# Optimization experiments

Measured on AMD Instinct MI355X. Metric: run time of the kernel, lower is better.

## Reference

```python
import jax, jax.numpy as jnp
import numpy as np

EPS = 1e-10


def _gcn(X, A, W, act):
    # A_hat = A + I; symmetric normalization D^{-1/2} A_hat D^{-1/2}
    N = A.shape[0]
    A_hat = A + jnp.eye(N, dtype=A.dtype)
    d = 1.0 / jnp.sqrt(jnp.sum(A_hat, axis=1) + EPS)
    A_norm = (d[:, None] * A_hat) * d[None, :]  # same math as diag @ A_hat @ diag
    return act(A_norm @ (X @ W))


def _pool(X, A, s, k):
    scores = (X @ s)[:, 0]            # [N]
    _, idx = jax.lax.top_k(scores, k)  # static k (ceil(ratio*N))
    return X[idx], A[idx][:, idx], idx


def _unpool(Xp, idx, N):
    return jnp.zeros((N, Xp.shape[-1]), Xp.dtype).at[idx].set(Xp)


def _glorot(key, shape):
    lim = np.sqrt(6.0 / (shape[0] + shape[1])).astype(np.float32)
    return jax.random.uniform(key, shape, jnp.float32, -lim, lim)


def setup_inputs() -> dict:
    key = jax.random.key(0)
    ks = jax.random.split(key, 8)
    N, F_IN, F, C = 8192, 16, 32, 2
    x = jax.random.normal(ks[0], (N, F_IN), jnp.float32)
    # sparse-ish symmetric binary adjacency stored densely (as the module expects)
    a = (jax.random.uniform(ks[1], (N, N)) < 0.01).astype(jnp.float32)
    a = jnp.maximum(a, a.T)
    return {
        "x": x,
        "a": a,
        "W1": _glorot(ks[2], (F_IN, F)),
        "W2": _glorot(ks[3], (F, F)),
        "W3": _glorot(ks[4], (F, F)),
        "W4": _glorot(ks[5], (F, C)),
        "s1": _glorot(ks[6], (F, 1)),
        "s2": _glorot(ks[7], (F, 1)),
    }


def reference(x, a, W1, W2, W3, W4, s1, s2):
    N = x.shape[0]
    K1 = int(np.ceil(0.5 * N))   # pool1 ratio 0.5
    K2 = int(np.ceil(0.5 * K1))  # pool2 ratio 0.5
    relu = jax.nn.relu
    X1 = _gcn(x, a, W1, relu)                     # [N, F]
    X1p, A1p, idx1 = _pool(X1, a, s1, K1)         # [K1, F], [K1, K1]
    X2 = _gcn(X1p, A1p, W2, relu)                 # [K1, F]
    X2p, _, idx2 = _pool(X2, A1p, s2, K2)         # [K2, F]
    X3 = _unpool(X2p, idx2, K1)                   # scatter back to [K1, F]
    X3 = _gcn(X3, A1p, W3, relu)
    X4 = _unpool(X3, idx1, N)                     # scatter back to [N, F]
    return _gcn(X4, a, W4, lambda z: jax.nn.softmax(z, axis=-1))
```

## Files before the change

kernel.cpp:

```cpp
#include <hip/hip_runtime.h>
#include <stdint.h>

#define NNODES 8192
#define KP1 4096
#define KP2 2048
#define FIN 16
#define FH 32
#define COUT 2
#define STRA 320
#define STRS 320
#define CGRID 1024
#define GRPSH 5
#define GRPSZ 32
#define BARWORDS (66 * 32)
#define RNONE 0xFFFFu

typedef unsigned short u16;
typedef unsigned int u32;

__global__ __launch_bounds__(256) void build_ell(const float* __restrict__ A, int n, int stride,
        u16* __restrict__ ell, int* __restrict__ rowcnt, int* __restrict__ diag, float* __restrict__ dnorm,
        const float* __restrict__ Xf, const float* __restrict__ Wf, float* __restrict__ Zf, int kf,
        u32* __restrict__ bar)
{
    if ((int)blockIdx.x >= n) {
        if ((int)blockIdx.x == n) {
            for (int w = threadIdx.x; w < BARWORDS; w += 256)
                __hip_atomic_store(&bar[w], 0u, __ATOMIC_RELAXED, __HIP_MEMORY_SCOPE_AGENT);
        }
        int t = ((int)blockIdx.x - n) * 256 + threadIdx.x;
        int i = t >> 5;
        int f = t & 31;
        const float* xr = Xf + (size_t)i * kf;
        float acc = 0.0f;
        for (int k = 0; k < kf; ++k) acc += xr[k] * Wf[k * 32 + f];
        Zf[t] = acc;
        return;
    }
    __shared__ int cnt;
    __shared__ int dg;
    int row = blockIdx.x;
    if (threadIdx.x == 0) { cnt = 0; dg = 0; }
    __syncthreads();
    const float4* arow4 = (const float4*)(A + (size_t)row * n);
    u16* erow = ell + (size_t)row * stride;
    int n4 = n >> 2;
    for (int c4 = threadIdx.x; c4 < n4; c4 += 256) {
        float4 v = arow4[c4];
        if (v.x == 0.0f && v.y == 0.0f && v.z == 0.0f && v.w == 0.0f) continue;
        int cb = c4 << 2;
        if (v.x != 0.0f) {
            if (cb == row) dg = 1;
            else { int p = atomicAdd(&cnt, 1); if (p < stride) erow[p] = (u16)cb; }
        }
        if (v.y != 0.0f) {
            int c = cb + 1;
            if (c == row) dg = 1;
            else { int p = atomicAdd(&cnt, 1); if (p < stride) erow[p] = (u16)c; }
        }
        if (v.z != 0.0f) {
            int c = cb + 2;
            if (c == row) dg = 1;
            else { int p = atomicAdd(&cnt, 1); if (p < stride) erow[p] = (u16)c; }
        }
        if (v.w != 0.0f) {
            int c = cb + 3;
            if (c == row) dg = 1;
            else { int p = atomicAdd(&cnt, 1); if (p < stride) erow[p] = (u16)c; }
        }
    }
    __syncthreads();
    if (threadIdx.x == 0) {
        int cf = cnt;
        rowcnt[row] = cf < stride ? cf : stride;
        diag[row] = dg;
        dnorm[row] = rsqrtf((float)(cf + dg + 1) + 1e-10f);
    }
}

__device__ __forceinline__ void gbar(u32* bar, int bid, int nblk)
{
    __syncthreads();
    if (threadIdx.x == 0) {
        __builtin_amdgcn_fence(__ATOMIC_RELEASE, "agent");
        int g = bid >> GRPSH;
        int ngrp = (nblk + GRPSZ - 1) >> GRPSH;
        int gsz = nblk - (g << GRPSH); if (gsz > GRPSZ) gsz = GRPSZ;
        u32* gcnt = bar + (size_t)g * 32;
        u32* ggen = bar + (size_t)(32 + g) * 32;
        u32* rcnt = bar + (size_t)64 * 32;
        u32* rgen = bar + (size_t)65 * 32;
        u32 sg = __hip_atomic_load(ggen, __ATOMIC_RELAXED, __HIP_MEMORY_SCOPE_AGENT);
        u32 a = __hip_atomic_fetch_add(gcnt, 1u, __ATOMIC_RELAXED, __HIP_MEMORY_SCOPE_AGENT);
        if (a == (u32)(gsz - 1)) {
            u32 sr = __hip_atomic_load(rgen, __ATOMIC_RELAXED, __HIP_MEMORY_SCOPE_AGENT);
            u32 r = __hip_atomic_fetch_add(rcnt, 1u, __ATOMIC_RELAXED, __HIP_MEMORY_SCOPE_AGENT);
            if (r == (u32)(ngrp - 1)) {
                __hip_atomic_store(rcnt, 0u, __ATOMIC_RELAXED, __HIP_MEMORY_SCOPE_AGENT);
                __hip_atomic_fetch_add(rgen, 1u, __ATOMIC_RELAXED, __HIP_MEMORY_SCOPE_AGENT);
            } else {
                while (__hip_atomic_load(rgen, __ATOMIC_RELAXED, __HIP_MEMORY_SCOPE_AGENT) == sr)
                    __builtin_amdgcn_s_sleep(2);
            }
            __hip_atomic_store(gcnt, 0u, __ATOMIC_RELAXED, __HIP_MEMORY_SCOPE_AGENT);
            __hip_atomic_fetch_add(ggen, 1u, __ATOMIC_RELAXED, __HIP_MEMORY_SCOPE_AGENT);
        } else {
            while (__hip_atomic_load(ggen, __ATOMIC_RELAXED, __HIP_MEMORY_SCOPE_AGENT) == sg)
                __builtin_amdgcn_s_sleep(4);
        }
        __builtin_amdgcn_fence(__ATOMIC_ACQUIRE, "agent");
    }
    __syncthreads();
}

struct TkS {
    u32 hist[4][256];
    u32 wsum[4];
    u32 pref;
    u32 rem;
};

__device__ __forceinline__ u32 km_of(float f)
{
    u32 u = __float_as_uint(f);
    u32 m;
    if (u & 0x80000000u) m = ~u; else m = u | 0x80000000u;
    return ~m;
}

__device__ void topk_local(TkS& s, u16* rank_l, u16* idx_l,
                           const float* __restrict__ scores, int n, int K, int tid,
                           int* __restrict__ grank, int* __restrict__ gidx, bool mirror)
{
    int wv = tid >> 6;
    int lane = tid & 63;
    int per = n >> 8;
    int base = tid * per;
    if (tid == 0) { s.pref = 0u; s.rem = (u32)K; }
    __syncthreads();
    for (int bp = 3; bp >= 0; --bp) {
        s.hist[0][tid] = 0u;
        s.hist[1][tid] = 0u;
        s.hist[2][tid] = 0u;
        s.hist[3][tid] = 0u;
        __syncthreads();
        u32 maskhi = 0u;
        if (bp < 3) maskhi = 0xFFFFFFFFu << ((bp + 1) * 8);
        u32 pref = s.pref;
        u32 rem = s.rem;
        for (int e = 0; e < per; ++e) {
            u32 km = km_of(scores[base + e]);
            if ((km & maskhi) == pref) atomicAdd(&s.hist[wv][(km >> (bp * 8)) & 255u], 1u);
        }
        __syncthreads();
        u32 tot = s.hist[0][tid] + s.hist[1][tid] + s.hist[2][tid] + s.hist[3][tid];
        u32 vv = tot;
        u32 t2;
        t2 = __shfl(vv, lane - 1);  if (lane >= 1)  vv += t2;
        t2 = __shfl(vv, lane - 2);  if (lane >= 2)  vv += t2;
        t2 = __shfl(vv, lane - 4);  if (lane >= 4)  vv += t2;
        t2 = __shfl(vv, lane - 8);  if (lane >= 8)  vv += t2;
        t2 = __shfl(vv, lane - 16); if (lane >= 16) vv += t2;
        t2 = __shfl(vv, lane - 32); if (lane >= 32) vv += t2;
        if (lane == 63) s.wsum[wv] = vv;
        __syncthreads();
        u32 add = 0u;
        if (wv > 0) add += s.wsum[0];
        if (wv > 1) add += s.wsum[1];
        if (wv > 2) add += s.wsum[2];
        u32 cum = vv + add;
        if (tot != 0u && cum >= rem && cum - tot < rem) {
            s.pref = pref | ((u32)tid << (bp * 8));
            s.rem = rem - (cum - tot);
        }
    }
    __syncthreads();
    u32 T = s.pref;
    u32 need_eq = s.rem;
    u32 run = 0u;
    for (int e = 0; e < per; ++e) {
        u32 km = km_of(scores[base + e]);
        if (km < T) run += 0x10000u;
        else if (km == T) run += 1u;
    }
    u32 v2 = run;
    u32 t3;
    t3 = __shfl(v2, lane - 1);  if (lane >= 1)  v2 += t3;
    t3 = __shfl(v2, lane - 2);  if (lane >= 2)  v2 += t3;
    t3 = __shfl(v2, lane - 4);  if (lane >= 4)  v2 += t3;
    t3 = __shfl(v2, lane - 8);  if (lane >= 8)  v2 += t3;
    t3 = __shfl(v2, lane - 16); if (lane >= 16) v2 += t3;
    t3 = __shfl(v2, lane - 32); if (lane >= 32) v2 += t3;
    if (lane == 63) s.wsum[wv] = v2;
    __syncthreads();
    u32 add2 = 0u;
    if (wv > 0) add2 += s.wsum[0];
    if (wv > 1) add2 += s.wsum[1];
    if (wv > 2) add2 += s.wsum[2];
    u32 cur = v2 + add2 - run;
    for (int e = 0; e < per; ++e) {
        int v = base + e;
        u32 km = km_of(scores[v]);
        u32 ltb = cur >> 16;
        u32 eqb = cur & 0xFFFFu;
        u32 eqs = eqb < need_eq ? eqb : need_eq;
        int sel = 0;
        if (km < T) { sel = 1; cur += 0x10000u; }
        else if (km == T) { if (eqb < need_eq) sel = 1; cur += 1u; }
        if (sel) {
            int r = (int)(ltb + eqs);
            rank_l[v] = (u16)r;
            idx_l[r] = (u16)v;
            if (mirror) { grank[v] = r; gidx[r] = v; }
        } else {
            rank_l[v] = RNONE;
            if (mirror) grank[v] = -1;
        }
    }
    __syncthreads();
}

template<bool REMAP, bool MASK, bool FW4, bool SC, bool EPI>
__device__ __forceinline__ void spmm_phase(
        const u16* __restrict__ ell, const int* __restrict__ rowcnt,
        const int* __restrict__ diag, const float* __restrict__ dnorm,
        const float* __restrict__ Z, const int* __restrict__ remap, const u16* mask_l,
        float* __restrict__ scores, const float* __restrict__ svec,
        const float* __restrict__ Wn, float* __restrict__ Zn,
        int n, int stride, int gwave, int nwaves, int lane)
{
    int g = lane >> 3;
    int q = lane & 7;
    for (int wid = gwave; wid < n; wid += nwaves) {
        int cnt = rowcnt[wid];
        const u16* erow = ell + (size_t)wid * stride;
        float ax = 0.0f, ay = 0.0f, az = 0.0f, aw = 0.0f;
        for (int it = g; it < cnt; it += 8) {
            int c = erow[it];
            if (MASK && mask_l[c] == RNONE) continue;
            int zc = REMAP ? remap[c] : c;
            float dn = dnorm[c];
            const float4* zp = (const float4*)(Z + (size_t)zc * 32);
            float4 zv = zp[q];
            ax += dn * zv.x;
            ay += dn * zv.y;
            az += dn * zv.z;
            aw += dn * zv.w;
        }
        ax += __shfl_xor(ax, 8);  ay += __shfl_xor(ay, 8);
        az += __shfl_xor(az, 8);  aw += __shfl_xor(aw, 8);
        ax += __shfl_xor(ax, 16); ay += __shfl_xor(ay, 16);
        az += __shfl_xor(az, 16); aw += __shfl_xor(aw, 16);
        ax += __shfl_xor(ax, 32); ay += __shfl_xor(ay, 32);
        az += __shfl_xor(az, 32); aw += __shfl_xor(aw, 32);
        float ox = 0.0f, oy = 0.0f, oz = 0.0f, ow = 0.0f;
        if (g == 0) {
            float dr = dnorm[wid];
            bool selfok = !(MASK && mask_l[wid] == RNONE);
            if (selfok) {
                int zc = REMAP ? remap[wid] : wid;
                const float4* zp = (const float4*)(Z + (size_t)zc * 32);
                float4 zv = zp[q];
                float cf = (float)(diag[wid] + 1) * dr;
                ax += cf * zv.x;
                ay += cf * zv.y;
                az += cf * zv.z;
                aw += cf * zv.w;
            }
            ox = fmaxf(dr * ax, 0.0f);
            oy = fmaxf(dr * ay, 0.0f);
            oz = fmaxf(dr * az, 0.0f);
            ow = fmaxf(dr * aw, 0.0f);
            if (FW4) {
                int kb = q * 4;
                float p0 = ox * Wn[(kb + 0) * 2 + 0] + oy * Wn[(kb + 1) * 2 + 0]
                         + oz * Wn[(kb + 2) * 2 + 0] + ow * Wn[(kb + 3) * 2 + 0];
                float p1 = ox * Wn[(kb + 0) * 2 + 1] + oy * Wn[(kb + 1) * 2 + 1]
                         + oz * Wn[(kb + 2) * 2 + 1] + ow * Wn[(kb + 3) * 2 + 1];
                p0 += __shfl_xor(p0, 1);
                p1 += __shfl_xor(p1, 1);
                p0 += __shfl_xor(p0, 2);
                p1 += __shfl_xor(p1, 2);
                p0 += __shfl_xor(p0, 4);
                p1 += __shfl_xor(p1, 4);
                if (q == 0) {
                    float2 r;
                    r.x = p0;
                    r.y = p1;
                    ((float2*)Zn)[wid] = r;
                }
            } else if (SC) {
                const float4* sp = (const float4*)svec;
                float4 sv = sp[q];
                float pp = ox * sv.x + oy * sv.y + oz * sv.z + ow * sv.w;
                pp += __shfl_xor(pp, 1);
                pp += __shfl_xor(pp, 2);
                pp += __shfl_xor(pp, 4);
                if (q == 0) scores[wid] = pp;
            }
        }
        if (EPI) {
            int f = lane & 31;
            float acc = 0.0f;
#pragma unroll
            for (int k = 0; k < 32; ++k) {
                float comp = ((k & 3) == 0) ? ox : ((k & 3) == 1) ? oy
                           : ((k & 3) == 2) ? oz : ow;
                float rowk = __shfl(comp, k >> 2);
                acc += rowk * Wn[k * 32 + f];
            }
            if (lane < 32) Zn[(size_t)wid * 32 + f] = acc;
        }
    }
}

__device__ __forceinline__ void subell_phase(const u16* __restrict__ ellA, const int* __restrict__ rowcntA,
        const int* __restrict__ diagA, const u16* idx_l, const u16* rank_l,
        u16* __restrict__ ellS, int* __restrict__ rowcntS, int* __restrict__ diagS, float* __restrict__ dnormS,
        int k1, int strideA, int strideS, int gwave, int nwaves, int lane)
{
    for (int wid = gwave; wid < k1; wid += nwaves) {
        int r = idx_l[wid];
        int cnt = rowcntA[r];
        const u16* erow = ellA + (size_t)r * strideA;
        u16* srow = ellS + (size_t)wid * strideS;
        int outn = 0;
        for (int t0 = 0; t0 < cnt; t0 += 64) {
            int it = t0 + lane;
            u16 rk = RNONE;
            if (it < cnt) rk = rank_l[erow[it]];
            unsigned long long b = __ballot(rk != RNONE);
            int ofs = __popcll(b & ((1ull << lane) - 1ull));
            if (rk != RNONE) srow[outn + ofs] = rk;
            outn += __popcll(b);
        }
        if (lane == 0) {
            int dg = diagA[r];
            rowcntS[wid] = outn;
            diagS[wid] = dg;
            dnormS[wid] = rsqrtf((float)(outn + dg + 1) + 1e-10f);
        }
    }
}

__device__ __forceinline__ void spmmout_phase(const u16* __restrict__ ell, const int* __restrict__ rowcnt,
        const int* __restrict__ diag, const float* __restrict__ dnorm, const float* __restrict__ Zr,
        const int* __restrict__ gat, float* __restrict__ out, int n, int stride,
        int gwave, int nwaves, int lane)
{
    const float2* Z2 = (const float2*)Zr;
    for (int wid = gwave; wid < n; wid += nwaves) {
        int cnt = rowcnt[wid];
        const u16* erow = ell + (size_t)wid * stride;
        float ax = 0.0f, ay = 0.0f;
        for (int it = lane; it < cnt; it += 64) {
            int c = erow[it];
            int rk = gat[c];
            if (rk >= 0) {
                float dn = dnorm[c];
                float2 zv = Z2[rk];
                ax += dn * zv.x;
                ay += dn * zv.y;
            }
        }
        ax += __shfl_xor(ax, 1);  ay += __shfl_xor(ay, 1);
        ax += __shfl_xor(ax, 2);  ay += __shfl_xor(ay, 2);
        ax += __shfl_xor(ax, 4);  ay += __shfl_xor(ay, 4);
        ax += __shfl_xor(ax, 8);  ay += __shfl_xor(ay, 8);
        ax += __shfl_xor(ax, 16); ay += __shfl_xor(ay, 16);
        ax += __shfl_xor(ax, 32); ay += __shfl_xor(ay, 32);
        if (lane == 0) {
            float dr = dnorm[wid];
            int rks = gat[wid];
            if (rks >= 0) {
                float cf = (float)(diag[wid] + 1) * dr;
                float2 zs = Z2[rks];
                ax += cf * zs.x;
                ay += cf * zs.y;
            }
            float v0 = dr * ax;
            float v1 = dr * ay;
            float m = fmaxf(v0, v1);
            float e0 = __expf(v0 - m);
            float e1 = __expf(v1 - m);
            float inv = 1.0f / (e0 + e1);
            float2 r;
            r.x = e0 * inv;
            r.y = e1 * inv;
            ((float2*)out)[wid] = r;
        }
    }
}

struct GcnP {
    const u16* ellA; const int* cntA; const int* diagA; const float* dnA;
    const float* Z1; float* sc1; int* rank1; int* idx1;
    u16* ellS; int* cntS; int* diagS; float* dnS;
    float* Z2f; float* sc2;
    float* Z3f; float* Z4r;
    const float* W2; const float* W3; const float* W4; const float* s1; const float* s2;
    float* out;
    u32* bar;
};

__global__ __launch_bounds__(256, 4) void gcn_pipeline(GcnP p)
{
    __shared__ TkS sm;
    __shared__ u16 rank_l[NNODES];
    __shared__ u16 idx_l[KP1];
    int tid = threadIdx.x;
    int bid = blockIdx.x;
    int lane = tid & 63;
    int gwave = (bid * 256 + tid) >> 6;
    int nwaves = ((int)gridDim.x * 256) >> 6;
    int nblk = (int)gridDim.x;

    spmm_phase<false, false, false, true, true>(p.ellA, p.cntA, p.diagA, p.dnA, p.Z1,
        (const int*)0, (const u16*)0, p.sc1, p.s1, p.W2, p.Z2f,
        NNODES, STRA, gwave, nwaves, lane);
    gbar(p.bar, bid, nblk);

    topk_local(sm, rank_l, idx_l, p.sc1, NNODES, KP1, tid, p.rank1, p.idx1, bid == 0);
    subell_phase(p.ellA, p.cntA, p.diagA, idx_l, rank_l, p.ellS, p.cntS, p.diagS, p.dnS,
        KP1, STRA, STRS, gwave, nwaves, lane);
    gbar(p.bar, bid, nblk);

    spmm_phase<true, false, false, true, true>(p.ellS, p.cntS, p.diagS, p.dnS, p.Z2f,
        p.idx1, (const u16*)0, p.sc2, p.s2, p.W3, p.Z3f,
        KP1, STRS, gwave, nwaves, lane);
    gbar(p.bar, bid, nblk);

    topk_local(sm, rank_l, idx_l, p.sc2, KP1, KP2, tid, (int*)0, (int*)0, false);
    spmm_phase<false, true, true, false, false>(p.ellS, p.cntS, p.diagS, p.dnS, p.Z3f,
        (const int*)0, rank_l, (float*)0, (const float*)0, p.W4, p.Z4r,
        KP1, STRS, gwave, nwaves, lane);
    gbar(p.bar, bid, nblk);

    spmmout_phase(p.ellA, p.cntA, p.diagA, p.dnA, p.Z4r, p.rank1, p.out,
        NNODES, STRA, gwave, nwaves, lane);
}

__global__ __launch_bounds__(256) void k_spmmA(const u16* __restrict__ ell, const int* __restrict__ rowcnt,
        const int* __restrict__ diag, const float* __restrict__ dnorm, const float* __restrict__ Z,
        float* __restrict__ scores, const float* __restrict__ svec,
        const float* __restrict__ Wn, float* __restrict__ Zn, int n, int stride)
{
    int gwave = ((int)blockIdx.x * 256 + (int)threadIdx.x) >> 6;
    int nwaves = ((int)gridDim.x * 256) >> 6;
    spmm_phase<false, false, false, true, true>(ell, rowcnt, diag, dnorm, Z,
        (const int*)0, (const u16*)0, scores, svec, Wn, Zn, n, stride, gwave, nwaves, threadIdx.x & 63);
}

__global__ __launch_bounds__(256) void k_phaseB(const float* __restrict__ scores,
        int* __restrict__ grank, int* __restrict__ gidx,
        const u16* __restrict__ ellA, const int* __restrict__ rowcntA, const int* __restrict__ diagA,
        u16* __restrict__ ellS, int* __restrict__ rowcntS, int* __restrict__ diagS, float* __restrict__ dnormS)
{
    __shared__ TkS sm;
    __shared__ u16 rank_l[NNODES];
    __shared__ u16 idx_l[KP1];
    int gwave = ((int)blockIdx.x * 256 + (int)threadIdx.x) >> 6;
    int nwaves = ((int)gridDim.x * 256) >> 6;
    topk_local(sm, rank_l, idx_l, scores, NNODES, KP1, threadIdx.x, grank, gidx, blockIdx.x == 0);
    subell_phase(ellA, rowcntA, diagA, idx_l, rank_l, ellS, rowcntS, diagS, dnormS,
        KP1, STRA, STRS, gwave, nwaves, threadIdx.x & 63);
}

__global__ __launch_bounds__(256) void k_spmmC(const u16* __restrict__ ell, const int* __restrict__ rowcnt,
        const int* __restrict__ diag, const float* __restrict__ dnorm, const float* __restrict__ Z,
        const int* __restrict__ remap, float* __restrict__ scores, const float* __restrict__ svec,
        const float* __restrict__ Wn, float* __restrict__ Zn, int n, int stride)
{
    int gwave = ((int)blockIdx.x * 256 + (int)threadIdx.x) >> 6;
    int nwaves = ((int)gridDim.x * 256) >> 6;
    spmm_phase<true, false, false, true, true>(ell, rowcnt, diag, dnorm, Z,
        remap, (const u16*)0, scores, svec, Wn, Zn, n, stride, gwave, nwaves, threadIdx.x & 63);
}

__global__ __launch_bounds__(256) void k_phaseD(const float* __restrict__ scores,
        const u16* __restrict__ ell, const int* __restrict__ rowcnt,
        const int* __restrict__ diag, const float* __restrict__ dnorm, const float* __restrict__ Z,
        const float* __restrict__ Wn, float* __restrict__ Zn, int n, int stride)
{
    __shared__ TkS sm;
    __shared__ u16 rank_l[NNODES];
    __shared__ u16 idx_l[KP1];
    int gwave = ((int)blockIdx.x * 256 + (int)threadIdx.x) >> 6;
    int nwaves = ((int)gridDim.x * 256) >> 6;
    topk_local(sm, rank_l, idx_l, scores, KP1, KP2, threadIdx.x, (int*)0, (int*)0, false);
    spmm_phase<false, true, true, false, false>(ell, rowcnt, diag, dnorm, Z,
        (const int*)0, rank_l, (float*)0, (const float*)0, Wn, Zn, n, stride, gwave, nwaves, threadIdx.x & 63);
}

__global__ __launch_bounds__(256) void k_spmmout(const u16* __restrict__ ell, const int* __restrict__ rowcnt,
        const int* __restrict__ diag, const float* __restrict__ dnorm, const float* __restrict__ Zr,
        const int* __restrict__ gat, float* __restrict__ out, int n, int stride)
{
    int gwave = ((int)blockIdx.x * 256 + (int)threadIdx.x) >> 6;
    int nwaves = ((int)gridDim.x * 256) >> 6;
    spmmout_phase(ell, rowcnt, diag, dnorm, Zr, gat, out, n, stride, gwave, nwaves, threadIdx.x & 63);
}

#define CARVE(type, name, bytes) \
    type name = (type)wp; wp += (((size_t)(bytes)) + 255) & ~((size_t)255);

extern "C" void kernel_launch(void* const* d_in, const int* in_sizes, int n_in,
                              void* d_out, int out_size, void* d_ws, size_t ws_size,
                              hipStream_t stream)
{
    const float* x  = (const float*)d_in[0];
    const float* a  = (const float*)d_in[1];
    const float* W1 = (const float*)d_in[2];
    const float* W2 = (const float*)d_in[3];
    const float* W3 = (const float*)d_in[4];
    const float* W4 = (const float*)d_in[5];
    const float* s1 = (const float*)d_in[6];
    const float* s2 = (const float*)d_in[7];
    float* out = (float*)d_out;
    (void)in_sizes; (void)n_in; (void)out_size; (void)ws_size;

    char* wp = (char*)d_ws;
    CARVE(u16*,   ellA,  (size_t)NNODES * STRA * sizeof(u16));
    CARVE(int*,   cntA,  NNODES * sizeof(int));
    CARVE(int*,   diagA, NNODES * sizeof(int));
    CARVE(float*, dnA,   NNODES * sizeof(float));
    CARVE(float*, Z1,    (size_t)NNODES * FH * sizeof(float));
    CARVE(float*, sc1,   NNODES * sizeof(float));
    CARVE(int*,   rank1, NNODES * sizeof(int));
    CARVE(int*,   idx1,  NNODES * sizeof(int));
    CARVE(u16*,   ellS,  (size_t)KP1 * STRS * sizeof(u16));
    CARVE(int*,   cntS,  KP1 * sizeof(int));
    CARVE(int*,   diagS, KP1 * sizeof(int));
    CARVE(float*, dnS,   KP1 * sizeof(float));
    CARVE(float*, Z2f,   (size_t)NNODES * FH * sizeof(float));
    CARVE(float*, sc2,   KP1 * sizeof(float));
    CARVE(float*, Z3f,   (size_t)KP1 * FH * sizeof(float));
    CARVE(float*, Z4r,   (size_t)KP1 * COUT * sizeof(float));
    CARVE(u32*,   barws, BARWORDS * sizeof(u32));

    build_ell<<<NNODES + (NNODES * FH) / 256, 256, 0, stream>>>(
        a, NNODES, STRA, ellA, cntA, diagA, dnA, x, W1, Z1, FIN, barws);

    static int g_ok = -1;
    if (g_ok < 0) {
        int maxb = 0;
        int ncu = 0;
        hipDeviceProp_t props;
        if (hipOccupancyMaxActiveBlocksPerMultiprocessor(&maxb, (const void*)gcn_pipeline, 256, 0)
                == hipSuccess
            && hipGetDeviceProperties(&props, 0) == hipSuccess)
            ncu = props.multiProcessorCount;
        g_ok = ((long)maxb * (long)ncu >= CGRID) ? 1 : 0;
    }

    if (g_ok) {
        GcnP pp;
        pp.ellA = ellA; pp.cntA = cntA; pp.diagA = diagA; pp.dnA = dnA;
        pp.Z1 = Z1; pp.sc1 = sc1; pp.rank1 = rank1; pp.idx1 = idx1;
        pp.ellS = ellS; pp.cntS = cntS; pp.diagS = diagS; pp.dnS = dnS;
        pp.Z2f = Z2f; pp.sc2 = sc2;
        pp.Z3f = Z3f; pp.Z4r = Z4r;
        pp.W2 = W2; pp.W3 = W3; pp.W4 = W4; pp.s1 = s1; pp.s2 = s2;
        pp.out = out;
        pp.bar = barws;
        gcn_pipeline<<<CGRID, 256, 0, stream>>>(pp);
    } else {
        k_spmmA<<<NNODES / 4, 256, 0, stream>>>(ellA, cntA, diagA, dnA, Z1,
            sc1, s1, W2, Z2f, NNODES, STRA);
        k_phaseB<<<KP1 / 4, 256, 0, stream>>>(sc1, rank1, idx1,
            ellA, cntA, diagA, ellS, cntS, diagS, dnS);
        k_spmmC<<<KP1 / 4, 256, 0, stream>>>(ellS, cntS, diagS, dnS, Z2f,
            idx1, sc2, s2, W3, Z3f, KP1, STRS);
        k_phaseD<<<KP1 / 4, 256, 0, stream>>>(sc2, ellS, cntS, diagS, dnS, Z3f,
            W4, Z4r, KP1, STRS);
        k_spmmout<<<NNODES / 4, 256, 0, stream>>>(ellA, cntA, diagA, dnA, Z4r, rank1, out, NNODES, STRA);
    }
}
```

Baseline: 498.3 us.

## Replace grid-barrier fences with agent-scope atomic stores and vmcnt wait

Removes the agent-scope release and acquire fences in the software grid barrier and replaces them with a plain s_waitcnt vmcnt(0). To keep cross-block data visible, all stores read by later phases become relaxed agent-scope atomic stores. The sub-ELL index array is widened from u16 to u32 so those stores can be atomic words. This trims cache writeback and invalidate costs at each barrier, but it doubles the sub-ELL index traffic and leans on loads not hitting stale non-coherent cache lines, which risks correctness.

Result: slower. 524.6 us (+5.3%).

```diff
diff --git a/kernel.cpp b/kernel.cpp
--- a/kernel.cpp
+++ b/kernel.cpp
@@ -17,6 +17,17 @@
 
 typedef unsigned short u16;
 typedef unsigned int u32;
+typedef unsigned long long u64;
+
+__device__ __forceinline__ void st_u32(void* p, u32 v)
+{
+    __hip_atomic_store((u32*)p, v, __ATOMIC_RELAXED, __HIP_MEMORY_SCOPE_AGENT);
+}
+__device__ __forceinline__ void st_f32(float* p, float v) { st_u32(p, __float_as_uint(v)); }
+__device__ __forceinline__ void st_u64(void* p, u64 v)
+{
+    __hip_atomic_store((u64*)p, v, __ATOMIC_RELAXED, __HIP_MEMORY_SCOPE_AGENT);
+}
 
 __global__ __launch_bounds__(256) void build_ell(const float* __restrict__ A, int n, int stride,
         u16* __restrict__ ell, int* __restrict__ rowcnt, int* __restrict__ diag, float* __restrict__ dnorm,
@@ -82,7 +93,7 @@
 {
     __syncthreads();
     if (threadIdx.x == 0) {
-        __builtin_amdgcn_fence(__ATOMIC_RELEASE, "agent");
+        asm volatile("s_waitcnt vmcnt(0)" ::: "memory");
         int g = bid >> GRPSH;
         int ngrp = (nblk + GRPSZ - 1) >> GRPSH;
         int gsz = nblk - (g << GRPSH); if (gsz > GRPSZ) gsz = GRPSZ;
@@ -108,7 +119,6 @@
             while (__hip_atomic_load(ggen, __ATOMIC_RELAXED, __HIP_MEMORY_SCOPE_AGENT) == sg)
                 __builtin_amdgcn_s_sleep(4);
         }
-        __builtin_amdgcn_fence(__ATOMIC_ACQUIRE, "agent");
     }
     __syncthreads();
 }
@@ -211,18 +221,18 @@
             int r = (int)(ltb + eqs);
             rank_l[v] = (u16)r;
             idx_l[r] = (u16)v;
-            if (mirror) { grank[v] = r; gidx[r] = v; }
+            if (mirror) { st_u32(&grank[v], (u32)r); st_u32(&gidx[r], (u32)v); }
         } else {
             rank_l[v] = RNONE;
-            if (mirror) grank[v] = -1;
-        }
-    }
-    __syncthreads();
-}
-
-template<bool REMAP, bool MASK, bool FW4, bool SC, bool EPI>
+            if (mirror) st_u32(&grank[v], 0xFFFFFFFFu);
+        }
+    }
+    __syncthreads();
+}
+
+template<typename ET, bool REMAP, bool MASK, bool FW4, bool SC, bool EPI>
 __device__ __forceinline__ void spmm_phase(
-        const u16* __restrict__ ell, const int* __restrict__ rowcnt,
+        const ET* __restrict__ ell, const int* __restrict__ rowcnt,
         const int* __restrict__ diag, const float* __restrict__ dnorm,
         const float* __restrict__ Z, const int* __restrict__ remap, const u16* mask_l,
         float* __restrict__ scores, const float* __restrict__ svec,
@@ -233,10 +243,10 @@
     int q = lane & 7;
     for (int wid = gwave; wid < n; wid += nwaves) {
         int cnt = rowcnt[wid];
-        const u16* erow = ell + (size_t)wid * stride;
+        const ET* erow = ell + (size_t)wid * stride;
         float ax = 0.0f, ay = 0.0f, az = 0.0f, aw = 0.0f;
         for (int it = g; it < cnt; it += 8) {
-            int c = erow[it];
+            int c = (int)erow[it];
             if (MASK && mask_l[c] == RNONE) continue;
             int zc = REMAP ? remap[c] : c;
             float dn = dnorm[c];
@@ -284,10 +294,10 @@
                 p0 += __shfl_xor(p0, 4);
                 p1 += __shfl_xor(p1, 4);
                 if (q == 0) {
-                    float2 r;
-                    r.x = p0;
-                    r.y = p1;
-                    ((float2*)Zn)[wid] = r;
+                    union { float2 f; u64 u; } cv;
+                    cv.f.x = p0;
+                    cv.f.y = p1;
+                    st_u64(&((float2*)Zn)[wid], cv.u);
                 }
             } else if (SC) {
                 const float4* sp = (const float4*)svec;
@@ -296,7 +306,7 @@
                 pp += __shfl_xor(pp, 1);
                 pp += __shfl_xor(pp, 2);
                 pp += __shfl_xor(pp, 4);
-                if (q == 0) scores[wid] = pp;
+                if (q == 0) st_f32(&scores[wid], pp);
             }
         }
         if (EPI) {
@@ -309,21 +319,21 @@
                 float rowk = __shfl(comp, k >> 2);
                 acc += rowk * Wn[k * 32 + f];
             }
-            if (lane < 32) Zn[(size_t)wid * 32 + f] = acc;
+            if (lane < 32) st_f32(&Zn[(size_t)wid * 32 + f], acc);
         }
     }
 }
 
 __device__ __forceinline__ void subell_phase(const u16* __restrict__ ellA, const int* __restrict__ rowcntA,
         const int* __restrict__ diagA, const u16* idx_l, const u16* rank_l,
-        u16* __restrict__ ellS, int* __restrict__ rowcntS, int* __restrict__ diagS, float* __restrict__ dnormS,
+        u32* __restrict__ ellS, int* __restrict__ rowcntS, int* __restrict__ diagS, float* __restrict__ dnormS,
         int k1, int strideA, int strideS, int gwave, int nwaves, int lane)
 {
     for (int wid = gwave; wid < k1; wid += nwaves) {
         int r = idx_l[wid];
         int cnt = rowcntA[r];
         const u16* erow = ellA + (size_t)r * strideA;
-        u16* srow = ellS + (size_t)wid * strideS;
+        u32* srow = ellS + (size_t)wid * strideS;
         int outn = 0;
         for (int t0 = 0; t0 < cnt; t0 += 64) {
             int it = t0 + lane;
@@ -331,14 +341,14 @@
             if (it < cnt) rk = rank_l[erow[it]];
             unsigned long long b = __ballot(rk != RNONE);
             int ofs = __popcll(b & ((1ull << lane) - 1ull));
-            if (rk != RNONE) srow[outn + ofs] = rk;
+            if (rk != RNONE) st_u32(&srow[outn + ofs], (u32)rk);
             outn += __popcll(b);
         }
         if (lane == 0) {
             int dg = diagA[r];
-            rowcntS[wid] = outn;
-            diagS[wid] = dg;
-            dnormS[wid] = rsqrtf((float)(outn + dg + 1) + 1e-10f);
+            st_u32(&rowcntS[wid], (u32)outn);
+            st_u32(&diagS[wid], (u32)dg);
+            st_f32(&dnormS[wid], rsqrtf((float)(outn + dg + 1) + 1e-10f));
         }
     }
 }
@@ -395,7 +405,7 @@
 struct GcnP {
     const u16* ellA; const int* cntA; const int* diagA; const float* dnA;
     const float* Z1; float* sc1; int* rank1; int* idx1;
-    u16* ellS; int* cntS; int* diagS; float* dnS;
+    u32* ellS; int* cntS; int* diagS; float* dnS;
     float* Z2f; float* sc2;
     float* Z3f; float* Z4r;
     const float* W2; const float* W3; const float* W4; const float* s1; const float* s2;
@@ -415,7 +425,7 @@
     int nwaves = ((int)gridDim.x * 256) >> 6;
     int nblk = (int)gridDim.x;
 
-    spmm_phase<false, false, false, true, true>(p.ellA, p.cntA, p.diagA, p.dnA, p.Z1,
+    spmm_phase<u16, false, false, false, true, true>(p.ellA, p.cntA, p.diagA, p.dnA, p.Z1,
         (const int*)0, (const u16*)0, p.sc1, p.s1, p.W2, p.Z2f,
         NNODES, STRA, gwave, nwaves, lane);
     gbar(p.bar, bid, nblk);
@@ -425,13 +435,13 @@
         KP1, STRA, STRS, gwave, nwaves, lane);
     gbar(p.bar, bid, nblk);
 
-    spmm_phase<true, false, false, true, true>(p.ellS, p.cntS, p.diagS, p.dnS, p.Z2f,
+    spmm_phase<u32, true, false, false, true, true>(p.ellS, p.cntS, p.diagS, p.dnS, p.Z2f,
         p.idx1, (const u16*)0, p.sc2, p.s2, p.W3, p.Z3f,
         KP1, STRS, gwave, nwaves, lane);
     gbar(p.bar, bid, nblk);
 
     topk_local(sm, rank_l, idx_l, p.sc2, KP1, KP2, tid, (int*)0, (int*)0, false);
-    spmm_phase<false, true, true, false, false>(p.ellS, p.cntS, p.diagS, p.dnS, p.Z3f,
+    spmm_phase<u32, false, true, true, false, false>(p.ellS, p.cntS, p.diagS, p.dnS, p.Z3f,
         (const int*)0, rank_l, (float*)0, (const float*)0, p.W4, p.Z4r,
         KP1, STRS, gwave, nwaves, lane);
     gbar(p.bar, bid, nblk);
@@ -447,14 +457,14 @@
 {
     int gwave = ((int)blockIdx.x * 256 + (int)threadIdx.x) >> 6;
     int nwaves = ((int)gridDim.x * 256) >> 6;
-    spmm_phase<false, false, false, true, true>(ell, rowcnt, diag, dnorm, Z,
+    spmm_phase<u16, false, false, false, true, true>(ell, rowcnt, diag, dnorm, Z,
         (const int*)0, (const u16*)0, scores, svec, Wn, Zn, n, stride, gwave, nwaves, threadIdx.x & 63);
 }
 
 __global__ __launch_bounds__(256) void k_phaseB(const float* __restrict__ scores,
         int* __restrict__ grank, int* __restrict__ gidx,
         const u16* __restrict__ ellA, const int* __restrict__ rowcntA, const int* __restrict__ diagA,
-        u16* __restrict__ ellS, int* __restrict__ rowcntS, int* __restrict__ diagS, float* __restrict__ dnormS)
+        u32* __restrict__ ellS, int* __restrict__ rowcntS, int* __restrict__ diagS, float* __restrict__ dnormS)
 {
     __shared__ TkS sm;
     __shared__ u16 rank_l[NNODES];
@@ -466,19 +476,19 @@
         KP1, STRA, STRS, gwave, nwaves, threadIdx.x & 63);
 }
 
-__global__ __launch_bounds__(256) void k_spmmC(const u16* __restrict__ ell, const int* __restrict__ rowcnt,
+__global__ __launch_bounds__(256) void k_spmmC(const u32* __restrict__ ell, const int* __restrict__ rowcnt,
         const int* __restrict__ diag, const float* __restrict__ dnorm, const float* __restrict__ Z,
         const int* __restrict__ remap, float* __restrict__ scores, const float* __restrict__ svec,
         const float* __restrict__ Wn, float* __restrict__ Zn, int n, int stride)
 {
     int gwave = ((int)blockIdx.x * 256 + (int)threadIdx.x) >> 6;
     int nwaves = ((int)gridDim.x * 256) >> 6;
-    spmm_phase<true, false, false, true, true>(ell, rowcnt, diag, dnorm, Z,
+    spmm_phase<u32, true, false, false, true, true>(ell, rowcnt, diag, dnorm, Z,
         remap, (const u16*)0, scores, svec, Wn, Zn, n, stride, gwave, nwaves, threadIdx.x & 63);
 }
 
 __global__ __launch_bounds__(256) void k_phaseD(const float* __restrict__ scores,
-        const u16* __restrict__ ell, const int* __restrict__ rowcnt,
+        const u32* __restrict__ ell, const int* __restrict__ rowcnt,
         const int* __restrict__ diag, const float* __restrict__ dnorm, const float* __restrict__ Z,
         const float* __restrict__ Wn, float* __restrict__ Zn, int n, int stride)
 {
@@ -488,7 +498,7 @@
     int gwave = ((int)blockIdx.x * 256 + (int)threadIdx.x) >> 6;
     int nwaves = ((int)gridDim.x * 256) >> 6;
     topk_local(sm, rank_l, idx_l, scores, KP1, KP2, threadIdx.x, (int*)0, (int*)0, false);
-    spmm_phase<false, true, true, false, false>(ell, rowcnt, diag, dnorm, Z,
+    spmm_phase<u32, false, true, true, false, false>(ell, rowcnt, diag, dnorm, Z,
         (const int*)0, rank_l, (float*)0, (const float*)0, Wn, Zn, n, stride, gwave, nwaves, threadIdx.x & 63);
 }
 
@@ -528,7 +538,7 @@
     CARVE(float*, sc1,   NNODES * sizeof(float));
     CARVE(int*,   rank1, NNODES * sizeof(int));
     CARVE(int*,   idx1,  NNODES * sizeof(int));
-    CARVE(u16*,   ellS,  (size_t)KP1 * STRS * sizeof(u16));
+    CARVE(u32*,   ellS,  (size_t)KP1 * STRS * sizeof(u32));
     CARVE(int*,   cntS,  KP1 * sizeof(int));
     CARVE(int*,   diagS, KP1 * sizeof(int));
     CARVE(float*, dnS,   KP1 * sizeof(float));
```
